# Kernel optimization log

Measured on AMD Instinct MI355X. Metric: run time of the kernel, lower is better.

## Reference

```python
import jax, jax.numpy as jnp
import numpy as np

B, S, E, H = 4, 1024, 1024, 16
HD = E // H  # 64


def setup_inputs() -> dict:
    key = jax.random.key(0)
    ks = jax.random.split(key, 9)
    scale = 1.0 / np.sqrt(E)
    x = jax.random.normal(ks[0], (B, S, E), dtype=jnp.float32)
    attention_mask = jnp.ones((B, S, S), dtype=jnp.int32)
    # per-head projection weights, batched over heads: [H, E, HD]
    Wq = jax.random.normal(ks[1], (H, E, HD), dtype=jnp.float32) * scale
    Wk = jax.random.normal(ks[2], (H, E, HD), dtype=jnp.float32) * scale
    Wv = jax.random.normal(ks[3], (H, E, HD), dtype=jnp.float32) * scale
    bq = jax.random.normal(ks[4], (H, HD), dtype=jnp.float32) * scale
    bk = jax.random.normal(ks[5], (H, HD), dtype=jnp.float32) * scale
    bv = jax.random.normal(ks[6], (H, HD), dtype=jnp.float32) * scale
    # output projection, torch Linear convention: [out_features, in_features]
    Wo = jax.random.normal(ks[7], (E, E), dtype=jnp.float32) * scale
    bo = jax.random.normal(ks[8], (E,), dtype=jnp.float32) * scale
    return {"x": x, "attention_mask": attention_mask, "Wq": Wq, "bq": bq,
            "Wk": Wk, "bk": bk, "Wv": Wv, "bv": bv, "Wo": Wo, "bo": bo}


def reference(x, attention_mask, Wq, bq, Wk, bk, Wv, bv, Wo, bo):
    # batched-over-heads QKV projections: (B,S,E) x (H,E,HD) -> (B,H,S,HD)
    q = jnp.einsum('bse,hed->bhsd', x, Wq) + bq[None, :, None, :]
    k = jnp.einsum('bse,hed->bhsd', x, Wk) + bk[None, :, None, :]
    v = jnp.einsum('bse,hed->bhsd', x, Wv) + bv[None, :, None, :]
    scores = jnp.einsum('bhsd,bhtd->bhst', q, k) / jnp.sqrt(jnp.float32(HD))
    mask = attention_mask[:, None, :, :]  # (B,1,S,S) broadcast over heads
    scores = jnp.where(mask == 0, -jnp.inf, scores)
    weights = jax.nn.softmax(scores, axis=-1)
    out = jnp.einsum('bhst,bhtd->bhsd', weights, v)
    # concat heads on last dim: (B,S,H*HD) == (B,S,E)
    out = out.transpose(0, 2, 1, 3).reshape(B, S, E)
    return out @ Wo.T + bo
```

## Files before the change

kernel.cpp:

```cpp
#include <hip/hip_runtime.h>
#include <hip/hip_bf16.h>

#define NB 4
#define SEQ 1024
#define EMB 1024
#define NH 16
#define HD 64

typedef unsigned short u16;
typedef __attribute__((ext_vector_type(8))) __bf16 bf16x8;
typedef __attribute__((ext_vector_type(8))) short short8;
typedef __attribute__((ext_vector_type(4))) float floatx4;

__device__ inline u16 f2b_rn(float f) {
    union { float f; unsigned int i; } x; x.f = f;
    unsigned int r = (x.i + 0x7FFFu + ((x.i >> 16) & 1u)) >> 16;
    return (u16)r;
}
__device__ inline bf16x8 s2b(short8 v) {
    union { short8 s; bf16x8 b; } x; x.s = v; return x.b;
}

__device__ inline void gload_lds16(const void* g, void* l) {
    __builtin_amdgcn_global_load_lds(
        (const __attribute__((address_space(1))) void*)g,
        (__attribute__((address_space(3))) void*)l, 16, 0, 0);
}

__device__ inline bf16x8 ldsfrag(const u16* base, int r, int c) {
    return s2b(*(const short8*)&base[r * 64 + (c ^ ((r & 7) * 8))]);
}

__device__ inline void cvt8(const float* __restrict__ s, u16* __restrict__ d) {
    float4 a = *(const float4*)(s);
    float4 b = *(const float4*)(s + 4);
    union { u16 u[8]; int4 v; } o;
    o.u[0] = f2b_rn(a.x); o.u[1] = f2b_rn(a.y); o.u[2] = f2b_rn(a.z); o.u[3] = f2b_rn(a.w);
    o.u[4] = f2b_rn(b.x); o.u[5] = f2b_rn(b.y); o.u[6] = f2b_rn(b.z); o.u[7] = f2b_rn(b.w);
    *(int4*)(d) = o.v;
}

__global__ __launch_bounds__(256) void prep(
    const float* __restrict__ x, const float* __restrict__ Wq,
    const float* __restrict__ Wk, const float* __restrict__ Wv,
    const int* __restrict__ mask,
    u16* __restrict__ xb, u16* __restrict__ Wt,
    unsigned long long* __restrict__ bits)
{
    __shared__ u16 T[64 * 80];
    int bx = blockIdx.x;
    int tid = threadIdx.x;

    if (bx < 512) {
        #pragma unroll
        for (int c = 0; c < 4; ++c) {
            int i = (bx * 4 + c) * 2048 + tid * 8;
            cvt8(x + i, xb + i);
        }
    } else if (bx < 1280) {
        int bx2 = bx - 512;
        int e0 = (bx2 & 15) * 64;
        int ph = bx2 >> 4;
        int p = ph >> 4, h = ph & 15;
        const float* W = (p == 0 ? Wq : (p == 1 ? Wk : Wv)) + h * (EMB * HD);
        #pragma unroll
        for (int c = 0; c < 2; ++c) {
            int flat = c * 2048 + tid * 8;
            int r = flat >> 6;
            int d = flat & 63;
            cvt8(W + (size_t)(e0 + r) * HD + d, &T[r * 80 + d]);
        }
        __syncthreads();
        int d = tid >> 2;
        int ec = tid & 3;
        union { u16 u[16]; int4 v[2]; } tmp;
        #pragma unroll
        for (int i = 0; i < 16; ++i) tmp.u[i] = T[(ec * 16 + i) * 80 + d];
        u16* dst = Wt + ((size_t)(p * NH + h) * HD + d) * EMB + e0 + ec * 16;
        *(int4*)(dst) = tmp.v[0];
        *(int4*)(dst + 8) = tmp.v[1];
    } else {
        int base = (bx - 1280) * 16 + (tid >> 6) * 4;
        int lane = tid & 63;
        #pragma unroll
        for (int i = 0; i < 4; ++i) {
            int gw = base + i;
            int m = mask[(size_t)gw * 64 + lane];
            unsigned long long bl = __ballot(m != 0);
            if (lane == 0) bits[gw] = bl;
        }
    }
}

#define BARX do { __builtin_amdgcn_sched_barrier(0); __builtin_amdgcn_s_barrier(); __builtin_amdgcn_sched_barrier(0); } while(0)
#define VMCNT6 asm volatile("s_waitcnt vmcnt(6)" ::: "memory")
#define VMCNT0 asm volatile("s_waitcnt vmcnt(0)" ::: "memory")

__device__ __forceinline__ void rd_b(const u16* B, int wn, int ln, int quad, bf16x8 (&bfr)[4][2]) {
    #pragma unroll
    for (int nc = 0; nc < 4; ++nc) {
        bfr[nc][0] = ldsfrag(B, wn * 64 + nc * 16 + ln, quad * 8);
        bfr[nc][1] = ldsfrag(B, wn * 64 + nc * 16 + ln, 32 + quad * 8);
    }
}
__device__ __forceinline__ void rd_a(const u16* A, int wm, int mf0, int ln, int quad, bf16x8 (&a)[2][2]) {
    #pragma unroll
    for (int jj = 0; jj < 2; ++jj) {
        a[jj][0] = ldsfrag(A, wm * 128 + (mf0 + jj) * 16 + ln, quad * 8);
        a[jj][1] = ldsfrag(A, wm * 128 + (mf0 + jj) * 16 + ln, 32 + quad * 8);
    }
}
__device__ __forceinline__ void mm8(floatx4 (&acc)[8][4], const bf16x8 (&a)[2][2],
                                    const bf16x8 (&bfr)[4][2], int mf0) {
    #pragma unroll
    for (int jj = 0; jj < 2; ++jj)
        #pragma unroll
        for (int nc = 0; nc < 4; ++nc) {
            acc[mf0 + jj][nc] = __builtin_amdgcn_mfma_f32_16x16x32_bf16(a[jj][0], bfr[nc][0], acc[mf0 + jj][nc], 0, 0, 0);
            acc[mf0 + jj][nc] = __builtin_amdgcn_mfma_f32_16x16x32_bf16(a[jj][1], bfr[nc][1], acc[mf0 + jj][nc], 0, 0, 0);
        }
}

#define STG(srcb, buf, c, kt) gload_lds16((srcb) + (size_t)(c) * 65536 + (kt) * 64 + soff, (buf) + (c) * 4096 + ldst)

__global__ __launch_bounds__(512, 2) void qkv_gemm(
    const u16* __restrict__ x,
    const u16* __restrict__ Wt2,
    const float* __restrict__ bq, const float* __restrict__ bk, const float* __restrict__ bv,
    u16* __restrict__ Q, u16* __restrict__ K, u16* __restrict__ Vt)
{
    __shared__ u16 L[65536];
    u16* A0s = L;
    u16* A1s = L + 16384;
    u16* B0s = L + 32768;
    u16* B1s = L + 49152;

    int gid = blockIdx.x;
    int xcd = gid & 7;
    int j   = gid >> 3;
    int mt_ = (xcd >> 1) * 4 + (j & 3);
    int nt_ = (xcd & 1) * 6 + (j >> 2);
    int m0 = mt_ * 256;
    int n0 = nt_ * 256;

    int tid = threadIdx.x;
    int w = tid >> 6, lane = tid & 63, quad = lane >> 4, ln = lane & 15;
    int wm = w >> 2, wn = w & 3;

    const u16* Asrc = x   + (size_t)m0 * EMB;
    const u16* Bsrc = Wt2 + (size_t)n0 * EMB;

    int sr = tid >> 3;
    int sc = ((tid & 7) ^ (sr & 7)) * 8;
    size_t soff = (size_t)sr * EMB + sc;
    int ldst = w * 512;

    STG(Asrc, A0s, 0, 0); STG(Asrc, A0s, 1, 0); STG(Asrc, A0s, 2, 0); STG(Asrc, A0s, 3, 0);
    STG(Bsrc, B0s, 0, 0); STG(Bsrc, B0s, 1, 0); STG(Bsrc, B0s, 2, 0); STG(Bsrc, B0s, 3, 0);
    STG(Bsrc, B1s, 0, 1); STG(Bsrc, B1s, 1, 1); STG(Bsrc, B1s, 2, 1); STG(Bsrc, B1s, 3, 1);
    STG(Asrc, A1s, 0, 1); STG(Asrc, A1s, 2, 1);
    VMCNT6;
    BARX;

    floatx4 acc[8][4] = {};
    bf16x8 bfr[4][2];
    bf16x8 a[2][2];

    for (int i = 0; i < 8; ++i) {
        const int T = 2 * i;
        const bool st = (i < 7);
        rd_b(B0s, wn, ln, quad, bfr);
        rd_a(A0s, wm, 0, ln, quad, a);
        STG(Asrc, A1s, 1, T + 1); STG(Asrc, A1s, 3, T + 1);
        BARX;
        __builtin_amdgcn_s_setprio(1); mm8(acc, a, bfr, 0); __builtin_amdgcn_s_setprio(0);
        BARX;
        rd_a(A0s, wm, 2, ln, quad, a);
        if (st) { STG(Bsrc, B0s, 0, T + 2); STG(Bsrc, B0s, 1, T + 2); }
        BARX;
        __builtin_amdgcn_s_setprio(1); mm8(acc, a, bfr, 2); __builtin_amdgcn_s_setprio(0);
        BARX;
        rd_a(A0s, wm, 4, ln, quad, a);
        if (st) { STG(Bsrc, B0s, 2, T + 2); STG(Bsrc, B0s, 3, T + 2); }
        BARX;
        __builtin_amdgcn_s_setprio(1); mm8(acc, a, bfr, 4); __builtin_amdgcn_s_setprio(0);
        BARX;
        rd_a(A0s, wm, 6, ln, quad, a);
        if (st) { STG(Asrc, A0s, 0, T + 2); STG(Asrc, A0s, 2, T + 2); }
        BARX;
        __builtin_amdgcn_s_setprio(1); mm8(acc, a, bfr, 6); __builtin_amdgcn_s_setprio(0);
        if (st) { VMCNT6; } else { VMCNT0; }
        BARX;
        rd_b(B1s, wn, ln, quad, bfr);
        rd_a(A1s, wm, 0, ln, quad, a);
        if (st) { STG(Asrc, A0s, 1, T + 2); STG(Asrc, A0s, 3, T + 2); }
        BARX;
        __builtin_amdgcn_s_setprio(1); mm8(acc, a, bfr, 0); __builtin_amdgcn_s_setprio(0);
        BARX;
        rd_a(A1s, wm, 2, ln, quad, a);
        if (st) { STG(Bsrc, B1s, 0, T + 3); STG(Bsrc, B1s, 1, T + 3); }
        BARX;
        __builtin_amdgcn_s_setprio(1); mm8(acc, a, bfr, 2); __builtin_amdgcn_s_setprio(0);
        BARX;
        rd_a(A1s, wm, 4, ln, quad, a);
        if (st) { STG(Bsrc, B1s, 2, T + 3); STG(Bsrc, B1s, 3, T + 3); }
        BARX;
        __builtin_amdgcn_s_setprio(1); mm8(acc, a, bfr, 4); __builtin_amdgcn_s_setprio(0);
        BARX;
        rd_a(A1s, wm, 6, ln, quad, a);
        if (st) { STG(Asrc, A1s, 0, T + 3); STG(Asrc, A1s, 2, T + 3); }
        BARX;
        __builtin_amdgcn_s_setprio(1); mm8(acc, a, bfr, 6); __builtin_amdgcn_s_setprio(0);
        if (st) { VMCNT6; }
        BARX;
    }

    int nbase = n0 + wn * 64;
    int p = nbase >> 10;
    int h = (nbase >> 6) & 15;
    const float* bias = (p == 0 ? bq : (p == 1 ? bk : bv));
    if (p < 2) {
        u16* Out = (p == 0) ? Q : K;
        float qs = (p == 0) ? 0.125f * 1.44269504f : 1.0f;
        #pragma unroll
        for (int nc = 0; nc < 4; ++nc) {
            int d = nc * 16 + ln;
            float bv_ = bias[(nbase & 1023) + d];
            #pragma unroll
            for (int mf = 0; mf < 8; ++mf) {
                #pragma unroll
                for (int reg = 0; reg < 4; ++reg) {
                    int m = m0 + wm * 128 + mf * 16 + quad * 4 + reg;
                    int b_ = m >> 10, s = m & 1023;
                    Out[((size_t)(b_ * NH + h) * SEQ + s) * HD + d] = f2b_rn((acc[mf][nc][reg] + bv_) * qs);
                }
            }
        }
    } else {
        #pragma unroll
        for (int nc = 0; nc < 4; ++nc) {
            int d = nc * 16 + ln;
            float bv_ = bias[(nbase & 1023) + d];
            #pragma unroll
            for (int mf = 0; mf < 8; ++mf) {
                int m = m0 + wm * 128 + mf * 16 + quad * 4;
                int b_ = m >> 10, s = m & 1023;
                union { u16 u[4]; uint2 v; } pk;
                #pragma unroll
                for (int reg = 0; reg < 4; ++reg)
                    pk.u[reg] = f2b_rn(acc[mf][nc][reg] + bv_);
                *(uint2*)&Vt[((size_t)(b_ * NH + h) * HD + d) * SEQ + s] = pk.v;
            }
        }
    }
}

__global__ __launch_bounds__(256) void attn(
    const u16* __restrict__ Q, const u16* __restrict__ K, const u16* __restrict__ Vt,
    const unsigned long long* __restrict__ bits,
    const float* __restrict__ Wo, u16* __restrict__ Wob,
    u16* __restrict__ Aout)
{
    const int PP = 72;
    __shared__ u16 Ks[64 * 64];
    __shared__ u16 Vs[80 * 64];
    __shared__ u16 Ps[128 * PP];

    int bid = blockIdx.x;
    int tid = threadIdx.x;

    if (bid >= 512) {
        int i = (bid - 512) * 2048 + tid * 8;
        cvt8(Wo + i, Wob + i);
        return;
    }

    int bh = bid & 63;
    int q0 = (bid >> 6) * 128;
    int b = bh >> 4, h = bh & 15;
    const u16* Qb = Q  + (size_t)bh * SEQ * HD;
    const u16* Kb = K  + (size_t)bh * SEQ * HD;
    const u16* Vb = Vt + (size_t)bh * HD * SEQ;

    int w = tid >> 6, lane = tid & 63, quad = lane >> 4, ln = lane & 15;

    if (tid < 16) *(uint2*)&Vs[64 * 64 + tid * 4] = make_uint2(0x3F803F80u, 0x3F803F80u);

    bf16x8 qf[2][2];
    #pragma unroll
    for (int s = 0; s < 2; ++s) {
        const u16* qp = Qb + (size_t)(q0 + w * 32 + s * 16 + ln) * HD + quad * 8;
        union { int4 i; bf16x8 b; } c0, c1;
        c0.i = *(const int4*)(qp);
        c1.i = *(const int4*)(qp + 32);
        qf[s][0] = c0.b; qf[s][1] = c1.b;
    }

    floatx4 o[2][5] = {};

    for (int tt = 0; tt < SEQ / 64; ++tt) {
        int t0 = tt * 64;
        __syncthreads();
        #pragma unroll
        for (int i = 0; i < 2; ++i) {
            int flat0 = i * 256 + (tid & 192);
            int flat = flat0 + lane;
            int r = flat >> 3;
            int c = ((flat & 7) ^ (r & 7)) * 8;
            gload_lds16(Kb + (size_t)(t0 + r) * HD + c, Ks + flat0 * 8);
            gload_lds16(Vb + (size_t)r * SEQ + t0 + c, Vs + flat0 * 8);
        }
        __syncthreads();

        floatx4 sc[2][4] = {};
        #pragma unroll
        for (int kk = 0; kk < 2; ++kk) {
            bf16x8 kf[4];
            #pragma unroll
            for (int tb = 0; tb < 4; ++tb)
                kf[tb] = ldsfrag(Ks, tb * 16 + ln, kk * 32 + quad * 8);
            #pragma unroll
            for (int s = 0; s < 2; ++s)
                #pragma unroll
                for (int tb = 0; tb < 4; ++tb)
                    sc[s][tb] = __builtin_amdgcn_mfma_f32_16x16x32_bf16(kf[tb], qf[s][kk], sc[s][tb], 0, 0, 0);
        }

        #pragma unroll
        for (int s = 0; s < 2; ++s) {
            unsigned long long bm = bits[((size_t)b * SEQ + q0 + w * 32 + s * 16 + ln) * 16 + tt];
            if (__any(bm != ~0ull)) {
                #pragma unroll
                for (int tb = 0; tb < 4; ++tb)
                    #pragma unroll
                    for (int reg = 0; reg < 4; ++reg)
                        if (!((bm >> (tb * 16 + quad * 4 + reg)) & 1)) sc[s][tb][reg] = -1e30f;
            }
        }

        #pragma unroll
        for (int s = 0; s < 2; ++s) {
            int mrow = w * 32 + s * 16 + ln;
            #pragma unroll
            for (int tb = 0; tb < 4; ++tb) {
                union { float f; unsigned int i; } e0_, e1_, e2_, e3_;
                e0_.f = __builtin_amdgcn_exp2f(sc[s][tb][0]);
                e1_.f = __builtin_amdgcn_exp2f(sc[s][tb][1]);
                e2_.f = __builtin_amdgcn_exp2f(sc[s][tb][2]);
                e3_.f = __builtin_amdgcn_exp2f(sc[s][tb][3]);
                uint2 pk;
                pk.x = ((e0_.i + 0x8000u) >> 16) | ((e1_.i + 0x8000u) & 0xFFFF0000u);
                pk.y = ((e2_.i + 0x8000u) >> 16) | ((e3_.i + 0x8000u) & 0xFFFF0000u);
                *(uint2*)&Ps[mrow * PP + tb * 16 + quad * 4] = pk;
            }
        }

        #pragma unroll
        for (int kk = 0; kk < 2; ++kk) {
            bf16x8 vf[5];
            #pragma unroll
            for (int dt = 0; dt < 5; ++dt)
                vf[dt] = ldsfrag(Vs, dt * 16 + ln, kk * 32 + quad * 8);
            #pragma unroll
            for (int s = 0; s < 2; ++s) {
                bf16x8 pf = s2b(*(const short8*)&Ps[(w * 32 + s * 16 + ln) * PP + kk * 32 + quad * 8]);
                #pragma unroll
                for (int dt = 0; dt < 5; ++dt)
                    o[s][dt] = __builtin_amdgcn_mfma_f32_16x16x32_bf16(pf, vf[dt], o[s][dt], 0, 0, 0);
            }
        }
    }

    #pragma unroll
    for (int s = 0; s < 2; ++s) {
        #pragma unroll
        for (int reg = 0; reg < 4; ++reg) {
            float l = __shfl(o[s][4][reg], lane & 48, 64);
            float inv = 1.0f / l;
            int m = q0 + w * 32 + s * 16 + quad * 4 + reg;
            #pragma unroll
            for (int dt = 0; dt < 4; ++dt)
                Aout[((size_t)b * SEQ + m) * EMB + h * HD + dt * 16 + ln] = f2b_rn(o[s][dt][reg] * inv);
        }
    }
}

__global__ __launch_bounds__(256) void out_proj(
    const u16* __restrict__ A,
    const u16* __restrict__ Wo,
    const float* __restrict__ bo,
    float* __restrict__ Out)
{
    __shared__ u16 As[64 * 64];
    __shared__ u16 Bs[128 * 64];

    int gid = blockIdx.x;
    int xcd = gid & 7;
    int j   = gid >> 3;
    int m0 = (xcd * 8 + (j & 7)) * 64;
    int n0 = (j >> 3) * 128;

    int tid = threadIdx.x;
    int w = tid >> 6, lane = tid & 63, quad = lane >> 4, ln = lane & 15;
    int wm = w & 1, wn = w >> 1;

    floatx4 acc[2][4] = {};

    for (int k0 = 0; k0 < EMB; k0 += 64) {
        __syncthreads();
        #pragma unroll
        for (int i = 0; i < 2; ++i) {
            int flat0 = i * 256 + (tid & 192);
            int flat = flat0 + lane;
            int r = flat >> 3;
            int c = ((flat & 7) ^ (r & 7)) * 8;
            gload_lds16(A + (size_t)(m0 + r) * EMB + k0 + c, As + flat0 * 8);
        }
        #pragma unroll
        for (int i = 0; i < 4; ++i) {
            int flat0 = i * 256 + (tid & 192);
            int flat = flat0 + lane;
            int r = flat >> 3;
            int c = ((flat & 7) ^ (r & 7)) * 8;
            gload_lds16(Wo + (size_t)(n0 + r) * EMB + k0 + c, Bs + flat0 * 8);
        }
        __syncthreads();

        #pragma unroll
        for (int kk = 0; kk < 2; ++kk) {
            bf16x8 a[2], bfr[4];
            #pragma unroll
            for (int mt = 0; mt < 2; ++mt)
                a[mt] = ldsfrag(As, wm * 32 + mt * 16 + ln, kk * 32 + quad * 8);
            #pragma unroll
            for (int nc = 0; nc < 4; ++nc)
                bfr[nc] = ldsfrag(Bs, wn * 64 + nc * 16 + ln, kk * 32 + quad * 8);
            #pragma unroll
            for (int mt = 0; mt < 2; ++mt)
                #pragma unroll
                for (int nc = 0; nc < 4; ++nc)
                    acc[mt][nc] = __builtin_amdgcn_mfma_f32_16x16x32_bf16(a[mt], bfr[nc], acc[mt][nc], 0, 0, 0);
        }
    }

    #pragma unroll
    for (int nc = 0; nc < 4; ++nc) {
        int n = n0 + wn * 64 + nc * 16 + ln;
        float bb = bo[n];
        #pragma unroll
        for (int mt = 0; mt < 2; ++mt) {
            #pragma unroll
            for (int reg = 0; reg < 4; ++reg) {
                int m = m0 + wm * 32 + mt * 16 + quad * 4 + reg;
                Out[(size_t)m * EMB + n] = acc[mt][nc][reg] + bb;
            }
        }
    }
}

extern "C" void kernel_launch(void* const* d_in, const int* in_sizes, int n_in,
                              void* d_out, int out_size, void* d_ws, size_t ws_size,
                              hipStream_t stream) {
    const float* x  = (const float*)d_in[0];
    const int*   mk = (const int*)d_in[1];
    const float* Wq = (const float*)d_in[2];
    const float* bq = (const float*)d_in[3];
    const float* Wk = (const float*)d_in[4];
    const float* bk = (const float*)d_in[5];
    const float* Wv = (const float*)d_in[6];
    const float* bv = (const float*)d_in[7];
    const float* Wo = (const float*)d_in[8];
    const float* bo = (const float*)d_in[9];
    float* out = (float*)d_out;

    const size_t MB = 1u << 20;
    char* ws = (char*)d_ws;
    u16* xb  = (u16*)ws;
    u16* Wt  = (u16*)(ws + 8 * MB);
    u16* Wob = (u16*)(ws + 14 * MB);
    unsigned long long* bits = (unsigned long long*)(ws + 16 * MB);
    u16* Qw  = (u16*)(ws + 16 * MB + 512 * 1024);
    u16* Kw  = (u16*)(ws + 24 * MB + 512 * 1024);
    u16* Vtw = (u16*)(ws + 32 * MB + 512 * 1024);
    u16* Ao  = xb;

    prep<<<5376, 256, 0, stream>>>(x, Wq, Wk, Wv, mk, xb, Wt, bits);
    qkv_gemm<<<192, 512, 0, stream>>>(xb, Wt, bq, bk, bv, Qw, Kw, Vtw);
    attn<<<1024, 256, 0, stream>>>(Qw, Kw, Vtw, bits, Wo, Wob, Ao);
    out_proj<<<512, 256, 0, stream>>>(Ao, Wob, bo, out);
}
```

Baseline: 185.5 us.

## Double-buffer K/V tiles in attention kernel with async prefetch

Splits the attention loop into a two-stage ping-pong over K/V LDS buffers. The next tile is issued via global_load_lds while the current one is computed, with manual vmcnt waits and barriers replacing the per-iteration load-then-sync. Mask bits are prefetched one tile ahead, and s_setprio is raised around the MFMA bursts. This adds LDS footprint and relies on hand-counted vmcnt values, where a miscount would cause races.

```diff
diff --git a/kernel.cpp b/kernel.cpp
--- a/kernel.cpp
+++ b/kernel.cpp
@@ -94,6 +94,7 @@
 
 #define BARX do { __builtin_amdgcn_sched_barrier(0); __builtin_amdgcn_s_barrier(); __builtin_amdgcn_sched_barrier(0); } while(0)
 #define VMCNT6 asm volatile("s_waitcnt vmcnt(6)" ::: "memory")
+#define VMCNT2 asm volatile("s_waitcnt vmcnt(2)" ::: "memory")
 #define VMCNT0 asm volatile("s_waitcnt vmcnt(0)" ::: "memory")
 
 __device__ __forceinline__ void rd_b(const u16* B, int wn, int ln, int quad, bf16x8 (&bfr)[4][2]) {
@@ -255,16 +256,101 @@
     }
 }
 
+__device__ __forceinline__ void astage(const u16* __restrict__ Kb, const u16* __restrict__ Vb,
+                                       u16* Kd, u16* Vd, int t0, int tid) {
+    #pragma unroll
+    for (int i = 0; i < 2; ++i) {
+        int flat0 = i * 256 + (tid & 192);
+        int flat = flat0 + (tid & 63);
+        int r = flat >> 3;
+        int c = ((flat & 7) ^ (r & 7)) * 8;
+        gload_lds16(Kb + (size_t)(t0 + r) * HD + c, Kd + flat0 * 8);
+        gload_lds16(Vb + (size_t)r * SEQ + t0 + c, Vd + flat0 * 8);
+    }
+}
+
+__device__ __forceinline__ void attn_tile(
+    const u16* Ksc, const u16* Vsc, u16* Ps,
+    const bf16x8 (&qf)[2][2], floatx4 (&o)[2][5],
+    unsigned long long bm0, unsigned long long bm1,
+    int w, int ln, int quad)
+{
+    const int PP = 72;
+    floatx4 sc[2][4] = {};
+    #pragma unroll
+    for (int kk = 0; kk < 2; ++kk) {
+        bf16x8 kf[4];
+        #pragma unroll
+        for (int tb = 0; tb < 4; ++tb)
+            kf[tb] = ldsfrag(Ksc, tb * 16 + ln, kk * 32 + quad * 8);
+        __builtin_amdgcn_s_setprio(1);
+        #pragma unroll
+        for (int s = 0; s < 2; ++s)
+            #pragma unroll
+            for (int tb = 0; tb < 4; ++tb)
+                sc[s][tb] = __builtin_amdgcn_mfma_f32_16x16x32_bf16(kf[tb], qf[s][kk], sc[s][tb], 0, 0, 0);
+        __builtin_amdgcn_s_setprio(0);
+    }
+
+    #pragma unroll
+    for (int s = 0; s < 2; ++s) {
+        unsigned long long bm = s ? bm1 : bm0;
+        if (__any(bm != ~0ull)) {
+            #pragma unroll
+            for (int tb = 0; tb < 4; ++tb)
+                #pragma unroll
+                for (int reg = 0; reg < 4; ++reg)
+                    if (!((bm >> (tb * 16 + quad * 4 + reg)) & 1)) sc[s][tb][reg] = -1e30f;
+        }
+    }
+
+    #pragma unroll
+    for (int s = 0; s < 2; ++s) {
+        int mrow = w * 32 + s * 16 + ln;
+        #pragma unroll
+        for (int tb = 0; tb < 4; ++tb) {
+            union { float f; unsigned int i; } e0_, e1_, e2_, e3_;
+            e0_.f = __builtin_amdgcn_exp2f(sc[s][tb][0]);
+            e1_.f = __builtin_amdgcn_exp2f(sc[s][tb][1]);
+            e2_.f = __builtin_amdgcn_exp2f(sc[s][tb][2]);
+            e3_.f = __builtin_amdgcn_exp2f(sc[s][tb][3]);
+            uint2 pk;
+            pk.x = ((e0_.i + 0x8000u) >> 16) | ((e1_.i + 0x8000u) & 0xFFFF0000u);
+            pk.y = ((e2_.i + 0x8000u) >> 16) | ((e3_.i + 0x8000u) & 0xFFFF0000u);
+            *(uint2*)&Ps[mrow * PP + tb * 16 + quad * 4] = pk;
+        }
+    }
+
+    #pragma unroll
+    for (int kk = 0; kk < 2; ++kk) {
+        bf16x8 vf[5];
+        #pragma unroll
+        for (int dt = 0; dt < 5; ++dt)
+            vf[dt] = ldsfrag(Vsc, dt * 16 + ln, kk * 32 + quad * 8);
+        #pragma unroll
+        for (int s = 0; s < 2; ++s) {
+            bf16x8 pf = s2b(*(const short8*)&Ps[(w * 32 + s * 16 + ln) * PP + kk * 32 + quad * 8]);
+            __builtin_amdgcn_s_setprio(1);
+            #pragma unroll
+            for (int dt = 0; dt < 5; ++dt)
+                o[s][dt] = __builtin_amdgcn_mfma_f32_16x16x32_bf16(pf, vf[dt], o[s][dt], 0, 0, 0);
+            __builtin_amdgcn_s_setprio(0);
+        }
+    }
+}
+
 __global__ __launch_bounds__(256) void attn(
     const u16* __restrict__ Q, const u16* __restrict__ K, const u16* __restrict__ Vt,
     const unsigned long long* __restrict__ bits,
     const float* __restrict__ Wo, u16* __restrict__ Wob,
     u16* __restrict__ Aout)
 {
-    const int PP = 72;
-    __shared__ u16 Ks[64 * 64];
-    __shared__ u16 Vs[80 * 64];
-    __shared__ u16 Ps[128 * PP];
+    __shared__ u16 L[16512 + 128 * 72];
+    u16* Ks0 = L;
+    u16* Ks1 = L + 4096;
+    u16* Vs0 = L + 8192;
+    u16* Vs1 = L + 12352;
+    u16* Ps  = L + 16512;
 
     int bid = blockIdx.x;
     int tid = threadIdx.x;
@@ -284,7 +370,10 @@
 
     int w = tid >> 6, lane = tid & 63, quad = lane >> 4, ln = lane & 15;
 
-    if (tid < 16) *(uint2*)&Vs[64 * 64 + tid * 4] = make_uint2(0x3F803F80u, 0x3F803F80u);
+    if (tid < 32) {
+        u16* dst = (tid < 16 ? L + 12288 : L + 16448) + (tid & 15) * 4;
+        *(uint2*)dst = make_uint2(0x3F803F80u, 0x3F803F80u);
+    }
 
     bf16x8 qf[2][2];
     #pragma unroll
@@ -296,79 +385,37 @@
         qf[s][0] = c0.b; qf[s][1] = c1.b;
     }
 
+    __syncthreads();
+
+    astage(Kb, Vb, Ks0, Vs0, 0,  tid);
+    astage(Kb, Vb, Ks1, Vs1, 64, tid);
+    size_t bb0 = ((size_t)b * SEQ + q0 + w * 32 + ln) * 16;
+    size_t bb1 = bb0 + 256;
+    unsigned long long bmn0 = bits[bb0];
+    unsigned long long bmn1 = bits[bb1];
+
     floatx4 o[2][5] = {};
 
-    for (int tt = 0; tt < SEQ / 64; ++tt) {
-        int t0 = tt * 64;
-        __syncthreads();
-        #pragma unroll
-        for (int i = 0; i < 2; ++i) {
-            int flat0 = i * 256 + (tid & 192);
-            int flat = flat0 + lane;
-            int r = flat >> 3;
-            int c = ((flat & 7) ^ (r & 7)) * 8;
-            gload_lds16(Kb + (size_t)(t0 + r) * HD + c, Ks + flat0 * 8);
-            gload_lds16(Vb + (size_t)r * SEQ + t0 + c, Vs + flat0 * 8);
-        }
-        __syncthreads();
-
-        floatx4 sc[2][4] = {};
-        #pragma unroll
-        for (int kk = 0; kk < 2; ++kk) {
-            bf16x8 kf[4];
-            #pragma unroll
-            for (int tb = 0; tb < 4; ++tb)
-                kf[tb] = ldsfrag(Ks, tb * 16 + ln, kk * 32 + quad * 8);
-            #pragma unroll
-            for (int s = 0; s < 2; ++s)
-                #pragma unroll
-                for (int tb = 0; tb < 4; ++tb)
-                    sc[s][tb] = __builtin_amdgcn_mfma_f32_16x16x32_bf16(kf[tb], qf[s][kk], sc[s][tb], 0, 0, 0);
-        }
-
-        #pragma unroll
-        for (int s = 0; s < 2; ++s) {
-            unsigned long long bm = bits[((size_t)b * SEQ + q0 + w * 32 + s * 16 + ln) * 16 + tt];
-            if (__any(bm != ~0ull)) {
-                #pragma unroll
-                for (int tb = 0; tb < 4; ++tb)
-                    #pragma unroll
-                    for (int reg = 0; reg < 4; ++reg)
-                        if (!((bm >> (tb * 16 + quad * 4 + reg)) & 1)) sc[s][tb][reg] = -1e30f;
-            }
-        }
-
-        #pragma unroll
-        for (int s = 0; s < 2; ++s) {
-            int mrow = w * 32 + s * 16 + ln;
-            #pragma unroll
-            for (int tb = 0; tb < 4; ++tb) {
-                union { float f; unsigned int i; } e0_, e1_, e2_, e3_;
-                e0_.f = __builtin_amdgcn_exp2f(sc[s][tb][0]);
-                e1_.f = __builtin_amdgcn_exp2f(sc[s][tb][1]);
-                e2_.f = __builtin_amdgcn_exp2f(sc[s][tb][2]);
-                e3_.f = __builtin_amdgcn_exp2f(sc[s][tb][3]);
-                uint2 pk;
-                pk.x = ((e0_.i + 0x8000u) >> 16) | ((e1_.i + 0x8000u) & 0xFFFF0000u);
-                pk.y = ((e2_.i + 0x8000u) >> 16) | ((e3_.i + 0x8000u) & 0xFFFF0000u);
-                *(uint2*)&Ps[mrow * PP + tb * 16 + quad * 4] = pk;
-            }
-        }
-
-        #pragma unroll
-        for (int kk = 0; kk < 2; ++kk) {
-            bf16x8 vf[5];
-            #pragma unroll
-            for (int dt = 0; dt < 5; ++dt)
-                vf[dt] = ldsfrag(Vs, dt * 16 + ln, kk * 32 + quad * 8);
-            #pragma unroll
-            for (int s = 0; s < 2; ++s) {
-                bf16x8 pf = s2b(*(const short8*)&Ps[(w * 32 + s * 16 + ln) * PP + kk * 32 + quad * 8]);
-                #pragma unroll
-                for (int dt = 0; dt < 5; ++dt)
-                    o[s][dt] = __builtin_amdgcn_mfma_f32_16x16x32_bf16(pf, vf[dt], o[s][dt], 0, 0, 0);
-            }
-        }
+    for (int i = 0; i < 8; ++i) {
+        VMCNT6;
+        BARX;
+        {
+            unsigned long long bc0 = bmn0, bc1 = bmn1;
+            bmn0 = bits[bb0 + (2 * i + 1)];
+            bmn1 = bits[bb1 + (2 * i + 1)];
+            attn_tile(Ks0, Vs0, Ps, qf, o, bc0, bc1, w, ln, quad);
+        }
+        BARX;
+        if (i < 7) astage(Kb, Vb, Ks0, Vs0, i * 128 + 128, tid);
+        if (i < 7) { VMCNT6; } else { VMCNT2; }
+        BARX;
+        {
+            unsigned long long bc0 = bmn0, bc1 = bmn1;
+            if (i < 7) { bmn0 = bits[bb0 + (2 * i + 2)]; bmn1 = bits[bb1 + (2 * i + 2)]; }
+            attn_tile(Ks1, Vs1, Ps, qf, o, bc0, bc1, w, ln, quad);
+        }
+        BARX;
+        if (i < 7) astage(Kb, Vb, Ks1, Vs1, i * 128 + 192, tid);
     }
 
     #pragma unroll
```

After: 184.7 us. No clear change (-0.4%).
